# Performance work log

Measured on AMD Instinct MI355X. Metric: run time of the kernel, lower is better.

The kernel has to match this reference:

```python
import jax, jax.numpy as jnp
import numpy as np

N_EMBD = 512
HEAD_SIZE = 64
B, T = 256, 256


def setup_inputs() -> dict:
    key = jax.random.key(0)
    ks = jax.random.split(key, 7)
    s = 1.0 / np.sqrt(N_EMBD)
    return {
        "x": jax.random.normal(ks[0], (B, T, N_EMBD), dtype=jnp.float32),
        "Wk": jax.random.uniform(ks[1], (N_EMBD, HEAD_SIZE), jnp.float32, -s, s),
        "bk": jax.random.uniform(ks[2], (HEAD_SIZE,), jnp.float32, -s, s),
        "Wq": jax.random.uniform(ks[3], (N_EMBD, HEAD_SIZE), jnp.float32, -s, s),
        "bq": jax.random.uniform(ks[4], (HEAD_SIZE,), jnp.float32, -s, s),
        "Wv": jax.random.uniform(ks[5], (N_EMBD, HEAD_SIZE), jnp.float32, -s, s),
        "bv": jax.random.uniform(ks[6], (HEAD_SIZE,), jnp.float32, -s, s),
    }


def reference(x, Wk, bk, Wq, bq, Wv, bv):
    # Single-head causal self-attention (dropout = identity in eval mode).
    Bq, Tq, C = x.shape
    k = x @ Wk + bk        # [B, T, H]
    q = x @ Wq + bq        # [B, T, H]
    v = x @ Wv + bv        # [B, T, H]
    scale = 1.0 / jnp.sqrt(jnp.asarray(k.shape[-1], x.dtype))
    scores = jnp.einsum('bth,bsh->bts', q, k) * scale  # [B, T, T]
    causal = jnp.tril(jnp.ones((Tq, Tq), dtype=bool))
    scores = jnp.where(causal, scores, -jnp.inf)
    attn = jax.nn.softmax(scores, axis=-1)
    return jnp.einsum('bts,bsh->bth', attn, v)  # [B, T, H]
```

## Files before the change

### kernel.cpp

```cpp
#include <hip/hip_runtime.h>
#include <stdint.h>

typedef __attribute__((ext_vector_type(8))) short bf16x8;
typedef __attribute__((ext_vector_type(4))) float f32x4;

#if __has_builtin(__builtin_amdgcn_exp2f)
#define EXP2F(x) __builtin_amdgcn_exp2f(x)
#else
#define EXP2F(x) exp2f(x)
#endif

__device__ __forceinline__ short f2bf(float f) {
    union { float f; uint32_t u; } c; c.f = f;
    return (short)((c.u + 0x7fffu + ((c.u >> 16) & 1u)) >> 16);
}

typedef __attribute__((address_space(1))) void gvoid;
typedef __attribute__((address_space(3))) void lvoid;
__device__ __forceinline__ void async_cp16(const void* g, void* l) {
    __builtin_amdgcn_global_load_lds((gvoid*)g, (lvoid*)l, 16, 0, 0);
}

__global__ void prep_kernel(const float* __restrict__ Wk, const float* __restrict__ bk,
                            const float* __restrict__ Wq, const float* __restrict__ bq,
                            const float* __restrict__ Wv, const float* __restrict__ bv,
                            short* __restrict__ Wt2g, float* __restrict__ bcat) {
    const int col = blockIdx.x;
    const float* W; const float* bb; int c0;
    if (col < 64)       { W = Wk; bb = bk; c0 = col; }
    else if (col < 128) { W = Wq; bb = bq; c0 = col - 64; }
    else                { W = Wv; bb = bv; c0 = col - 128; }
    for (int c = threadIdx.x; c < 512; c += blockDim.x)
        Wt2g[(c >> 5) * (192 * 32) + col * 32 + (c & 31)] = f2bf(W[(size_t)c * 64 + c0]);
    if (threadIdx.x == 0) bcat[col] = bb[c0];
}

#define PSTR 40

__global__ __launch_bounds__(1024, 4) void fused_kernel(
    const float* __restrict__ x, const short* __restrict__ Wt2g,
    const float* __restrict__ bcat, float* __restrict__ out) {
    extern __shared__ __align__(16) char smem[];

    const int tid = threadIdx.x;
    const int wave = tid >> 6, lane = tid & 63;
    const int quad = lane >> 4, l16 = lane & 15;
    const int b = blockIdx.x;
    const int t = wave;

    f32x4 acc[12];
#pragma unroll
    for (int i = 0; i < 12; i++) acc[i] = (f32x4){0.f, 0.f, 0.f, 0.f};

    const int xr = lane >> 3;
    const int xsl = lane & 7;

#define STAGE_X(kc, bufp)                                                           \
    for (int g = 0; g < 2; g++) {                                                   \
        const int i = wave + g * 16;                                                \
        const int r = i * 8 + xr;                                                   \
        const int s = xsl ^ ((r & 3) << 1);                                         \
        async_cp16(x + ((size_t)b * 256 + r) * 512 + (kc) * 32 + s * 4,             \
                   smem + (bufp) * 32768 + i * 1024);                               \
    }
#define STAGE_W(kc, bufp)                                                           \
    if (wave < 12) {                                                                \
        async_cp16(Wt2g + (size_t)(kc) * 6144 + wave * 512 + lane * 8,              \
                   smem + 65536 + (bufp) * 12288 + wave * 1024);                    \
    }

    STAGE_X(0, 0)
    STAGE_W(0, 0)
    __syncthreads();

    const int axoff = (quad ^ (l16 & 3)) * 8;
    const int arow = t * 16 + l16;
    for (int kc = 0; kc < 16; kc++) {
        const int buf = kc & 1;
        if (kc < 15) { STAGE_X(kc + 1, buf ^ 1) STAGE_W(kc + 1, buf ^ 1) }
        const float* xa = (const float*)(smem + buf * 32768) + arow * 32 + axoff;
        f32x4 u0 = *(const f32x4*)xa, u1 = *(const f32x4*)(xa + 4);
        bf16x8 a;
#pragma unroll
        for (int i = 0; i < 4; i++) { a[i] = f2bf(u0[i]); a[4 + i] = f2bf(u1[i]); }
        const short* wb = (const short*)(smem + 65536 + buf * 12288);
#pragma unroll
        for (int nt = 0; nt < 12; nt++) {
            bf16x8 bfrag = *(const bf16x8*)&wb[(nt * 16 + l16) * 32 + quad * 8];
            acc[nt] = __builtin_amdgcn_mfma_f32_16x16x32_bf16(a, bfrag, acc[nt], 0, 0, 0);
        }
        __syncthreads();
    }

    short* Ks  = (short*)smem;
    short* Qs  = (short*)(smem + 32768);
    short* Vts = (short*)(smem + 65536);
    short* Ps  = (short*)(smem + 98304);
#pragma unroll
    for (int nt = 0; nt < 12; nt++) {
        const int col = nt * 16 + l16;
        const float bias = bcat[col];
        const int h = col & 63;
#pragma unroll
        for (int r = 0; r < 4; r++) {
            const short v = f2bf(acc[nt][r] + bias);
            const int row = t * 16 + quad * 4 + r;
            if (nt < 4)
                Ks[row * 64 + (((h >> 3) ^ (row & 7)) << 3) + (h & 7)] = v;
            else if (nt < 8)
                Qs[row * 64 + (((h >> 3) ^ (row & 7)) << 3) + (h & 7)] = v;
            else
                Vts[h * 256 + (((row >> 3) ^ (h & 7)) << 3) + (row & 7)] = v;
        }
    }
    __syncthreads();

    const float sc2 = 0.125f * 1.44269504088896340736f;
    short* myP = Ps + wave * (16 * PSTR);

    const int qrow = t * 16 + l16;
    const int sw = l16 & 7;
    bf16x8 qf0 = *(const bf16x8*)&Qs[qrow * 64 + ((quad ^ sw) << 3)];
    bf16x8 qf1 = *(const bf16x8*)&Qs[qrow * 64 + (((4 + quad) ^ sw) << 3)];

    f32x4 St[16];
#pragma unroll
    for (int i = 0; i < 16; i++) St[i] = (f32x4){0.f, 0.f, 0.f, 0.f};
#pragma unroll
    for (int nt = 0; nt < 16; nt++) if (nt <= t) {
        const int krow = nt * 16 + l16;
        bf16x8 kf0 = *(const bf16x8*)&Ks[krow * 64 + ((quad ^ sw) << 3)];
        bf16x8 kf1 = *(const bf16x8*)&Ks[krow * 64 + (((4 + quad) ^ sw) << 3)];
        St[nt] = __builtin_amdgcn_mfma_f32_16x16x32_bf16(qf0, kf0, St[nt], 0, 0, 0);
        St[nt] = __builtin_amdgcn_mfma_f32_16x16x32_bf16(qf1, kf1, St[nt], 0, 0, 0);
    }

    const int rowq = t * 16 + quad * 4;
    float mx[4], ls[4];
#pragma unroll
    for (int r = 0; r < 4; r++) mx[r] = -3.0e38f;
#pragma unroll
    for (int nt = 0; nt < 16; nt++) if (nt <= t) {
        const int cs = nt * 16 + l16;
#pragma unroll
        for (int r = 0; r < 4; r++) {
            float s = (cs <= rowq + r) ? St[nt][r] * sc2 : -3.0e38f;
            St[nt][r] = s;
            mx[r] = fmaxf(mx[r], s);
        }
    }
#pragma unroll
    for (int d = 1; d < 16; d <<= 1)
#pragma unroll
        for (int r = 0; r < 4; r++)
            mx[r] = fmaxf(mx[r], __shfl_xor(mx[r], d, 64));
#pragma unroll
    for (int r = 0; r < 4; r++) ls[r] = 0.f;
#pragma unroll
    for (int nt = 0; nt < 16; nt++) if (nt <= t) {
#pragma unroll
        for (int r = 0; r < 4; r++) {
            float p = EXP2F(St[nt][r] - mx[r]);
            St[nt][r] = p;
            ls[r] += p;
        }
    }
#pragma unroll
    for (int d = 1; d < 16; d <<= 1)
#pragma unroll
        for (int r = 0; r < 4; r++)
            ls[r] += __shfl_xor(ls[r], d, 64);

    f32x4 O[4];
#pragma unroll
    for (int i = 0; i < 4; i++) O[i] = (f32x4){0.f, 0.f, 0.f, 0.f};
    const int nch = (t + 2) >> 1;
#pragma unroll
    for (int c2 = 0; c2 < 8; c2++) if (c2 < nch) {
#pragma unroll
        for (int t2i = 0; t2i < 2; t2i++) {
            const int nt = c2 * 2 + t2i;
#pragma unroll
            for (int r = 0; r < 4; r++)
                myP[(quad * 4 + r) * PSTR + t2i * 16 + l16] = f2bf(St[nt][r]);
        }
        bf16x8 pf = *(const bf16x8*)&myP[l16 * PSTR + quad * 8];
#pragma unroll
        for (int ht = 0; ht < 4; ht++) {
            const int h = ht * 16 + l16;
            bf16x8 vf = *(const bf16x8*)&Vts[h * 256 + (((c2 * 4 + quad) ^ (h & 7)) << 3)];
            O[ht] = __builtin_amdgcn_mfma_f32_16x16x32_bf16(pf, vf, O[ht], 0, 0, 0);
        }
    }

    float rls[4];
#pragma unroll
    for (int r = 0; r < 4; r++) rls[r] = 1.0f / ls[r];
#pragma unroll
    for (int ht = 0; ht < 4; ht++)
#pragma unroll
        for (int r = 0; r < 4; r++)
            out[((size_t)b * 256 + rowq + r) * 64 + ht * 16 + l16] = O[ht][r] * rls[r];
#undef STAGE_X
#undef STAGE_W
}

extern "C" void kernel_launch(void* const* d_in, const int* in_sizes, int n_in,
                              void* d_out, int out_size, void* d_ws, size_t ws_size,
                              hipStream_t stream) {
    const float* x  = (const float*)d_in[0];
    const float* Wk = (const float*)d_in[1];
    const float* bk = (const float*)d_in[2];
    const float* Wq = (const float*)d_in[3];
    const float* bq = (const float*)d_in[4];
    const float* Wv = (const float*)d_in[5];
    const float* bv = (const float*)d_in[6];
    float* out = (float*)d_out;

    char* ws = (char*)d_ws;
    short* Wt2g = (short*)(ws);
    float* bcat = (float*)(ws + 196608);

    const int smem_bytes = 118784;
    (void)hipFuncSetAttribute((const void*)fused_kernel,
                              hipFuncAttributeMaxDynamicSharedMemorySize, smem_bytes);

    prep_kernel<<<192, 256, 0, stream>>>(Wk, bk, Wq, bq, Wv, bv, Wt2g, bcat);
    fused_kernel<<<256, 1024, smem_bytes, stream>>>(x, Wt2g, bcat, out);
}
```

Before: 216.7 us.

## Retile QKV projection into 64x48 per-wave blocks with register-staged bf16 x

The projection GEMM is reorganised so each wave computes a 64-row by 48-column tile (4x3 MFMA accumulators) instead of 16 rows by all 192 columns. The cut in redundant W fragment loads from LDS per MFMA is meant to improve operand reuse. x is now loaded from global into registers, converted to bf16 once and stored to LDS, halving x LDS footprint and removing per-wave repeated conversion, but replacing the async global-to-LDS copy with synchronous register loads. The attention phase permutes query tiles across waves to balance causal work within SIMD groups.

```diff
diff --git a/kernel.cpp b/kernel.cpp
--- a/kernel.cpp
+++ b/kernel.cpp
@@ -46,48 +46,58 @@
     const int wave = tid >> 6, lane = tid & 63;
     const int quad = lane >> 4, l16 = lane & 15;
     const int b = blockIdx.x;
-    const int t = wave;
-
-    f32x4 acc[12];
-#pragma unroll
-    for (int i = 0; i < 12; i++) acc[i] = (f32x4){0.f, 0.f, 0.f, 0.f};
-
-    const int xr = lane >> 3;
-    const int xsl = lane & 7;
-
-#define STAGE_X(kc, bufp)                                                           \
-    for (int g = 0; g < 2; g++) {                                                   \
-        const int i = wave + g * 16;                                                \
-        const int r = i * 8 + xr;                                                   \
-        const int s = xsl ^ ((r & 3) << 1);                                         \
-        async_cp16(x + ((size_t)b * 256 + r) * 512 + (kc) * 32 + s * 4,             \
-                   smem + (bufp) * 32768 + i * 1024);                               \
-    }
+
+    const int rg = wave >> 2, cg = wave & 3;
+
+    f32x4 acc[4][3];
+#pragma unroll
+    for (int m = 0; m < 4; m++)
+#pragma unroll
+        for (int j = 0; j < 3; j++) acc[m][j] = (f32x4){0.f, 0.f, 0.f, 0.f};
+
+    const float* xg = x + ((size_t)b * 256 + wave * 16 + l16) * 512 + quad * 8;
+
 #define STAGE_W(kc, bufp)                                                           \
     if (wave < 12) {                                                                \
         async_cp16(Wt2g + (size_t)(kc) * 6144 + wave * 512 + lane * 8,              \
-                   smem + 65536 + (bufp) * 12288 + wave * 1024);                    \
-    }
-
-    STAGE_X(0, 0)
+                   smem + 32768 + (bufp) * 12288 + wave * 1024);                    \
+    }
+
     STAGE_W(0, 0)
+    f32x4 xr0 = *(const f32x4*)xg;
+    f32x4 xr1 = *(const f32x4*)(xg + 4);
+    {
+        bf16x8 v;
+#pragma unroll
+        for (int i = 0; i < 4; i++) { v[i] = f2bf(xr0[i]); v[4 + i] = f2bf(xr1[i]); }
+        *(bf16x8*)((short*)smem + wave * 512 + lane * 8) = v;
+    }
     __syncthreads();
 
-    const int axoff = (quad ^ (l16 & 3)) * 8;
-    const int arow = t * 16 + l16;
     for (int kc = 0; kc < 16; kc++) {
         const int buf = kc & 1;
-        if (kc < 15) { STAGE_X(kc + 1, buf ^ 1) STAGE_W(kc + 1, buf ^ 1) }
-        const float* xa = (const float*)(smem + buf * 32768) + arow * 32 + axoff;
-        f32x4 u0 = *(const f32x4*)xa, u1 = *(const f32x4*)(xa + 4);
-        bf16x8 a;
-#pragma unroll
-        for (int i = 0; i < 4; i++) { a[i] = f2bf(u0[i]); a[4 + i] = f2bf(u1[i]); }
-        const short* wb = (const short*)(smem + 65536 + buf * 12288);
-#pragma unroll
-        for (int nt = 0; nt < 12; nt++) {
-            bf16x8 bfrag = *(const bf16x8*)&wb[(nt * 16 + l16) * 32 + quad * 8];
-            acc[nt] = __builtin_amdgcn_mfma_f32_16x16x32_bf16(a, bfrag, acc[nt], 0, 0, 0);
+        if (kc < 15) {
+            STAGE_W(kc + 1, buf ^ 1)
+            xr0 = *(const f32x4*)(xg + (kc + 1) * 32);
+            xr1 = *(const f32x4*)(xg + (kc + 1) * 32 + 4);
+        }
+        const short* wb = (const short*)(smem + 32768 + buf * 12288);
+        bf16x8 bfr0 = *(const bf16x8*)&wb[(cg * 48 + l16) * 32 + quad * 8];
+        bf16x8 bfr1 = *(const bf16x8*)&wb[(cg * 48 + 16 + l16) * 32 + quad * 8];
+        bf16x8 bfr2 = *(const bf16x8*)&wb[(cg * 48 + 32 + l16) * 32 + quad * 8];
+        const short* xbr = (const short*)smem + buf * 8192;
+#pragma unroll
+        for (int m = 0; m < 4; m++) {
+            bf16x8 afr = *(const bf16x8*)&xbr[(rg * 4 + m) * 512 + lane * 8];
+            acc[m][0] = __builtin_amdgcn_mfma_f32_16x16x32_bf16(afr, bfr0, acc[m][0], 0, 0, 0);
+            acc[m][1] = __builtin_amdgcn_mfma_f32_16x16x32_bf16(afr, bfr1, acc[m][1], 0, 0, 0);
+            acc[m][2] = __builtin_amdgcn_mfma_f32_16x16x32_bf16(afr, bfr2, acc[m][2], 0, 0, 0);
+        }
+        if (kc < 15) {
+            bf16x8 v;
+#pragma unroll
+            for (int i = 0; i < 4; i++) { v[i] = f2bf(xr0[i]); v[4 + i] = f2bf(xr1[i]); }
+            *(bf16x8*)((short*)smem + (buf ^ 1) * 8192 + wave * 512 + lane * 8) = v;
         }
         __syncthreads();
     }
@@ -97,28 +107,33 @@
     short* Vts = (short*)(smem + 65536);
     short* Ps  = (short*)(smem + 98304);
 #pragma unroll
-    for (int nt = 0; nt < 12; nt++) {
-        const int col = nt * 16 + l16;
+    for (int j = 0; j < 3; j++) {
+        const int col = cg * 48 + j * 16 + l16;
         const float bias = bcat[col];
         const int h = col & 63;
-#pragma unroll
-        for (int r = 0; r < 4; r++) {
-            const short v = f2bf(acc[nt][r] + bias);
-            const int row = t * 16 + quad * 4 + r;
-            if (nt < 4)
-                Ks[row * 64 + (((h >> 3) ^ (row & 7)) << 3) + (h & 7)] = v;
-            else if (nt < 8)
-                Qs[row * 64 + (((h >> 3) ^ (row & 7)) << 3) + (h & 7)] = v;
-            else
-                Vts[h * 256 + (((row >> 3) ^ (h & 7)) << 3) + (row & 7)] = v;
+        const int sel = col >> 6;
+#pragma unroll
+        for (int m = 0; m < 4; m++) {
+#pragma unroll
+            for (int r = 0; r < 4; r++) {
+                const short v = f2bf(acc[m][j][r] + bias);
+                const int row = rg * 64 + m * 16 + quad * 4 + r;
+                if (sel == 0)
+                    Ks[row * 64 + (((h >> 3) ^ (row & 7)) << 3) + (h & 7)] = v;
+                else if (sel == 1)
+                    Qs[row * 64 + (((h >> 3) ^ (row & 7)) << 3) + (h & 7)] = v;
+                else
+                    Vts[h * 256 + (((row >> 3) ^ (h & 7)) << 3) + (row & 7)] = v;
+            }
         }
     }
     __syncthreads();
 
+    const int qt = ((wave >> 2) << 2) | ((wave & 3) ^ (wave >> 2));
     const float sc2 = 0.125f * 1.44269504088896340736f;
     short* myP = Ps + wave * (16 * PSTR);
 
-    const int qrow = t * 16 + l16;
+    const int qrow = qt * 16 + l16;
     const int sw = l16 & 7;
     bf16x8 qf0 = *(const bf16x8*)&Qs[qrow * 64 + ((quad ^ sw) << 3)];
     bf16x8 qf1 = *(const bf16x8*)&Qs[qrow * 64 + (((4 + quad) ^ sw) << 3)];
@@ -127,7 +142,7 @@
 #pragma unroll
     for (int i = 0; i < 16; i++) St[i] = (f32x4){0.f, 0.f, 0.f, 0.f};
 #pragma unroll
-    for (int nt = 0; nt < 16; nt++) if (nt <= t) {
+    for (int nt = 0; nt < 16; nt++) if (nt <= qt) {
         const int krow = nt * 16 + l16;
         bf16x8 kf0 = *(const bf16x8*)&Ks[krow * 64 + ((quad ^ sw) << 3)];
         bf16x8 kf1 = *(const bf16x8*)&Ks[krow * 64 + (((4 + quad) ^ sw) << 3)];
@@ -135,12 +150,12 @@
         St[nt] = __builtin_amdgcn_mfma_f32_16x16x32_bf16(qf1, kf1, St[nt], 0, 0, 0);
     }
 
-    const int rowq = t * 16 + quad * 4;
+    const int rowq = qt * 16 + quad * 4;
     float mx[4], ls[4];
 #pragma unroll
     for (int r = 0; r < 4; r++) mx[r] = -3.0e38f;
 #pragma unroll
-    for (int nt = 0; nt < 16; nt++) if (nt <= t) {
+    for (int nt = 0; nt < 16; nt++) if (nt <= qt) {
         const int cs = nt * 16 + l16;
 #pragma unroll
         for (int r = 0; r < 4; r++) {
@@ -157,7 +172,7 @@
 #pragma unroll
     for (int r = 0; r < 4; r++) ls[r] = 0.f;
 #pragma unroll
-    for (int nt = 0; nt < 16; nt++) if (nt <= t) {
+    for (int nt = 0; nt < 16; nt++) if (nt <= qt) {
 #pragma unroll
         for (int r = 0; r < 4; r++) {
             float p = EXP2F(St[nt][r] - mx[r]);
@@ -174,7 +189,7 @@
     f32x4 O[4];
 #pragma unroll
     for (int i = 0; i < 4; i++) O[i] = (f32x4){0.f, 0.f, 0.f, 0.f};
-    const int nch = (t + 2) >> 1;
+    const int nch = (qt + 2) >> 1;
 #pragma unroll
     for (int c2 = 0; c2 < 8; c2++) if (c2 < nch) {
 #pragma unroll
@@ -201,7 +216,6 @@
 #pragma unroll
         for (int r = 0; r < 4; r++)
             out[((size_t)b * 256 + rowq + r) * 64 + ht * 16 + l16] = O[ht][r] * rls[r];
-#undef STAGE_X
 #undef STAGE_W
 }
 
```

Result: slower. 222.0 us (+2.4%).

## Load projection operands directly from global memory and rebalance causal tiles across SIMDs

Applied to the files above, without the earlier changes.

The QKV projection no longer stages x and W tiles into LDS with async copies and per-iteration barriers. Each lane now reads its MFMA fragments straight from global memory, with a one-step register prefetch of x, and the 12 W fragments per k-chunk come from L2/L1. Separately, the query-tile-to-wave mapping is permuted so causal attention work (which grows with the tile index) is spread more evenly across the four SIMDs. This trades LDS staging and sync overhead for more scattered global and cache traffic, since every wave re-reads all of W.

```diff
diff --git a/kernel.cpp b/kernel.cpp
--- a/kernel.cpp
+++ b/kernel.cpp
@@ -13,12 +13,6 @@
 __device__ __forceinline__ short f2bf(float f) {
     union { float f; uint32_t u; } c; c.f = f;
     return (short)((c.u + 0x7fffu + ((c.u >> 16) & 1u)) >> 16);
-}
-
-typedef __attribute__((address_space(1))) void gvoid;
-typedef __attribute__((address_space(3))) void lvoid;
-__device__ __forceinline__ void async_cp16(const void* g, void* l) {
-    __builtin_amdgcn_global_load_lds((gvoid*)g, (lvoid*)l, 16, 0, 0);
 }
 
 __global__ void prep_kernel(const float* __restrict__ Wk, const float* __restrict__ bk,
@@ -31,7 +25,7 @@
     else if (col < 128) { W = Wq; bb = bq; c0 = col - 64; }
     else                { W = Wv; bb = bv; c0 = col - 128; }
     for (int c = threadIdx.x; c < 512; c += blockDim.x)
-        Wt2g[(c >> 5) * (192 * 32) + col * 32 + (c & 31)] = f2bf(W[(size_t)c * 64 + c0]);
+        Wt2g[(c >> 5) * 6144 + col * 32 + (c & 31)] = f2bf(W[(size_t)c * 64 + c0]);
     if (threadIdx.x == 0) bcat[col] = bb[c0];
 }
 
@@ -52,44 +46,27 @@
 #pragma unroll
     for (int i = 0; i < 12; i++) acc[i] = (f32x4){0.f, 0.f, 0.f, 0.f};
 
-    const int xr = lane >> 3;
-    const int xsl = lane & 7;
-
-#define STAGE_X(kc, bufp)                                                           \
-    for (int g = 0; g < 2; g++) {                                                   \
-        const int i = wave + g * 16;                                                \
-        const int r = i * 8 + xr;                                                   \
-        const int s = xsl ^ ((r & 3) << 1);                                         \
-        async_cp16(x + ((size_t)b * 256 + r) * 512 + (kc) * 32 + s * 4,             \
-                   smem + (bufp) * 32768 + i * 1024);                               \
-    }
-#define STAGE_W(kc, bufp)                                                           \
-    if (wave < 12) {                                                                \
-        async_cp16(Wt2g + (size_t)(kc) * 6144 + wave * 512 + lane * 8,              \
-                   smem + 65536 + (bufp) * 12288 + wave * 1024);                    \
-    }
-
-    STAGE_X(0, 0)
-    STAGE_W(0, 0)
-    __syncthreads();
-
-    const int axoff = (quad ^ (l16 & 3)) * 8;
-    const int arow = t * 16 + l16;
+    const float* xg = x + ((size_t)b * 256 + t * 16 + l16) * 512 + quad * 8;
+    const short* wg = Wt2g + l16 * 32 + quad * 8;
+
+    f32x4 u0 = *(const f32x4*)xg;
+    f32x4 u1 = *(const f32x4*)(xg + 4);
     for (int kc = 0; kc < 16; kc++) {
-        const int buf = kc & 1;
-        if (kc < 15) { STAGE_X(kc + 1, buf ^ 1) STAGE_W(kc + 1, buf ^ 1) }
-        const float* xa = (const float*)(smem + buf * 32768) + arow * 32 + axoff;
-        f32x4 u0 = *(const f32x4*)xa, u1 = *(const f32x4*)(xa + 4);
+        f32x4 n0, n1;
+        if (kc < 15) {
+            n0 = *(const f32x4*)(xg + (kc + 1) * 32);
+            n1 = *(const f32x4*)(xg + (kc + 1) * 32 + 4);
+        }
         bf16x8 a;
 #pragma unroll
         for (int i = 0; i < 4; i++) { a[i] = f2bf(u0[i]); a[4 + i] = f2bf(u1[i]); }
-        const short* wb = (const short*)(smem + 65536 + buf * 12288);
+        const short* wk = wg + kc * 6144;
 #pragma unroll
         for (int nt = 0; nt < 12; nt++) {
-            bf16x8 bfrag = *(const bf16x8*)&wb[(nt * 16 + l16) * 32 + quad * 8];
-            acc[nt] = __builtin_amdgcn_mfma_f32_16x16x32_bf16(a, bfrag, acc[nt], 0, 0, 0);
-        }
-        __syncthreads();
+            bf16x8 bf = *(const bf16x8*)(wk + nt * 512);
+            acc[nt] = __builtin_amdgcn_mfma_f32_16x16x32_bf16(a, bf, acc[nt], 0, 0, 0);
+        }
+        u0 = n0; u1 = n1;
     }
 
     short* Ks  = (short*)smem;
@@ -115,10 +92,11 @@
     }
     __syncthreads();
 
+    const int qt = ((wave >> 2) << 2) | ((wave & 3) ^ (wave >> 2));
     const float sc2 = 0.125f * 1.44269504088896340736f;
     short* myP = Ps + wave * (16 * PSTR);
 
-    const int qrow = t * 16 + l16;
+    const int qrow = qt * 16 + l16;
     const int sw = l16 & 7;
     bf16x8 qf0 = *(const bf16x8*)&Qs[qrow * 64 + ((quad ^ sw) << 3)];
     bf16x8 qf1 = *(const bf16x8*)&Qs[qrow * 64 + (((4 + quad) ^ sw) << 3)];
@@ -127,7 +105,7 @@
 #pragma unroll
     for (int i = 0; i < 16; i++) St[i] = (f32x4){0.f, 0.f, 0.f, 0.f};
 #pragma unroll
-    for (int nt = 0; nt < 16; nt++) if (nt <= t) {
+    for (int nt = 0; nt < 16; nt++) if (nt <= qt) {
         const int krow = nt * 16 + l16;
         bf16x8 kf0 = *(const bf16x8*)&Ks[krow * 64 + ((quad ^ sw) << 3)];
         bf16x8 kf1 = *(const bf16x8*)&Ks[krow * 64 + (((4 + quad) ^ sw) << 3)];
@@ -135,12 +113,12 @@
         St[nt] = __builtin_amdgcn_mfma_f32_16x16x32_bf16(qf1, kf1, St[nt], 0, 0, 0);
     }
 
-    const int rowq = t * 16 + quad * 4;
+    const int rowq = qt * 16 + quad * 4;
     float mx[4], ls[4];
 #pragma unroll
     for (int r = 0; r < 4; r++) mx[r] = -3.0e38f;
 #pragma unroll
-    for (int nt = 0; nt < 16; nt++) if (nt <= t) {
+    for (int nt = 0; nt < 16; nt++) if (nt <= qt) {
         const int cs = nt * 16 + l16;
 #pragma unroll
         for (int r = 0; r < 4; r++) {
@@ -157,7 +135,7 @@
 #pragma unroll
     for (int r = 0; r < 4; r++) ls[r] = 0.f;
 #pragma unroll
-    for (int nt = 0; nt < 16; nt++) if (nt <= t) {
+    for (int nt = 0; nt < 16; nt++) if (nt <= qt) {
 #pragma unroll
         for (int r = 0; r < 4; r++) {
             float p = EXP2F(St[nt][r] - mx[r]);
@@ -174,7 +152,7 @@
     f32x4 O[4];
 #pragma unroll
     for (int i = 0; i < 4; i++) O[i] = (f32x4){0.f, 0.f, 0.f, 0.f};
-    const int nch = (t + 2) >> 1;
+    const int nch = (qt + 2) >> 1;
 #pragma unroll
     for (int c2 = 0; c2 < 8; c2++) if (c2 < nch) {
 #pragma unroll
@@ -201,8 +179,6 @@
 #pragma unroll
         for (int r = 0; r < 4; r++)
             out[((size_t)b * 256 + rowq + r) * 64 + ht * 16 + l16] = O[ht][r] * rls[r];
-#undef STAGE_X
-#undef STAGE_W
 }
 
 extern "C" void kernel_launch(void* const* d_in, const int* in_sizes, int n_in,
```

Result: slower. 235.4 us (+8.6%).
